# Performance work log

Hardware: AMD Instinct MI355X
Metric: run time of the kernel (lower is better)

The kernel has to match this reference:

```python
import jax, jax.numpy as jnp
import numpy as np

N = 50000
E = 800000
NEG_SLOPE = 0.2


def gat_layer(x, src, dst, W, al, ar):
    # x: [N, F_in]; W: [F_in, H*D]; al/ar: [H, D]
    H, D = al.shape
    feat = (x @ W).reshape(N, H, D)                      # [N, H, D]
    el = jnp.einsum('nhd,hd->nh', feat, al)              # [N, H]
    er = jnp.einsum('nhd,hd->nh', feat, ar)              # [N, H]
    e = jax.nn.leaky_relu(el[src] + er[dst], NEG_SLOPE)  # [E, H]
    # segment softmax over edges grouped by destination node
    m = jax.ops.segment_max(e, dst, num_segments=N)      # [N, H] (-inf for empty)
    a = jnp.exp(e - m[dst])                              # [E, H]
    s = jax.ops.segment_sum(a, dst, num_segments=N)      # [N, H]
    a = a / jnp.where(s[dst] > 0, s[dst], 1.0)
    # weighted gather-aggregate of messages
    out = jax.ops.segment_sum(a[:, :, None] * feat[src], dst, num_segments=N)
    return out                                           # [N, H, D]


def setup_inputs() -> dict:
    key = jax.random.key(0)
    ks = jax.random.split(key, 9)
    in_size, hid, out_size = 512, 64, 64
    H1, H2 = 4, 4
    return {
        'x':   jax.random.normal(ks[0], (N, in_size), dtype=jnp.float32),
        'src': jax.random.randint(ks[1], (E,), 0, N, dtype=jnp.int32),
        'dst': jax.random.randint(ks[2], (E,), 0, N, dtype=jnp.int32),
        'W1':  jax.random.normal(ks[3], (in_size, H1 * hid), dtype=jnp.float32) * 0.05,
        'al1': jax.random.normal(ks[4], (H1, hid), dtype=jnp.float32) * 0.1,
        'ar1': jax.random.normal(ks[5], (H1, hid), dtype=jnp.float32) * 0.1,
        'W2':  jax.random.normal(ks[6], (H1 * hid, H2 * out_size), dtype=jnp.float32) * 0.05,
        'al2': jax.random.normal(ks[7], (H2, out_size), dtype=jnp.float32) * 0.1,
        'ar2': jax.random.normal(ks[8], (H2, out_size), dtype=jnp.float32) * 0.1,
    }


def reference(x, src, dst, W1, al1, ar1, W2, al2, ar2):
    h = gat_layer(x, src, dst, W1, al1, ar1)   # [N, H1, hid]
    h = jax.nn.elu(h).reshape(N, -1)           # flatten heads -> [N, H1*hid]
    h = gat_layer(h, src, dst, W2, al2, ar2)   # [N, H2, out]
    return h.mean(axis=1)                      # mean over heads -> [N, out]
```

## Files before the change

### kernel.cpp

```cpp
#include <hip/hip_runtime.h>

#define NNODES 50000
#define NEDGES 800000
#define HH 4
#define DD 64
#define FEAT 256
#define MPAD 50048
#define NB 196
#define GB (MPAD / 128)
#define SB1 ((NEDGES + 511) / 512)
#define BCAP 128

typedef __attribute__((ext_vector_type(8))) _Float16 frag16;
typedef __attribute__((ext_vector_type(4))) float frag_cd;
typedef __attribute__((ext_vector_type(4))) _Float16 h4v;
typedef __attribute__((ext_vector_type(8))) _Float16 h8v;

__global__ __launch_bounds__(256) void front0_kernel(
    int* __restrict__ cnt, const float* __restrict__ W1,
    const float* __restrict__ W2, _Float16* __restrict__ Bp1,
    _Float16* __restrict__ Bp2) {
  int b = blockIdx.x;
  if (b < NB) {
    int i = b * 256 + threadIdx.x;
    if (i < NNODES) cnt[i] = 0;
  } else {
    int idx = (b - NB) * 256 + threadIdx.x;
    if (idx < 512 * 256) {
      int k = idx >> 8, n = idx & 255;
      Bp1[(size_t)n * 512 + k] = (_Float16)W1[idx];
    } else {
      idx -= 512 * 256;
      int k = idx >> 8, n = idx & 255;
      Bp2[(size_t)n * 256 + k] = (_Float16)W2[idx];
    }
  }
}

template <int AF32>
__device__ __forceinline__ void gemm_body(
    const void* __restrict__ Av, const _Float16* __restrict__ Bp,
    _Float16* __restrict__ featb, const float* __restrict__ al,
    const float* __restrict__ ar, float* __restrict__ elp,
    float* __restrict__ erp, int M, int K, int bid,
    _Float16* __restrict__ As, _Float16* __restrict__ Bs) {
  const int tid = threadIdx.x;
  const int w = tid >> 6, lane = tid & 63;
  const int q = lane >> 4, ln = lane & 15;
  const int rowBase = bid * 128;
  const int wm = (w >> 2) * 64;
  const int wn = (w & 3) * 64;

  frag_cd acc[4][4] = {};

  const int nt = K >> 6;
  const int srow8 = lane >> 3;
  const int scg = ((lane & 7) ^ srow8) * 8;
  const int sw = ln & 7;

  const int ar_ = tid >> 2, aq = tid & 3;
  const int as0 = ((aq * 2) ^ (ar_ & 7)) * 8;
  const int as1 = ((aq * 2 + 1) ^ (ar_ & 7)) * 8;
  const int xrow = rowBase + ar_;

  const float* __restrict__ x = (const float*)Av;
  const _Float16* __restrict__ Ap = (const _Float16*)Av;

  for (int t = 0; t < nt; ++t) {
    const int kk = t << 6;
    __syncthreads();

    if constexpr (AF32) {
      float4 v0, v1, v2, v3;
      v0 = v1 = v2 = v3 = make_float4(0.f, 0.f, 0.f, 0.f);
      if (xrow < M) {
        const float4* xp = (const float4*)(x + (size_t)xrow * 512 + kk + aq * 16);
        v0 = xp[0]; v1 = xp[1]; v2 = xp[2]; v3 = xp[3];
      }
      frag16 f0, f1;
      f0[0] = (_Float16)v0.x; f0[1] = (_Float16)v0.y;
      f0[2] = (_Float16)v0.z; f0[3] = (_Float16)v0.w;
      f0[4] = (_Float16)v1.x; f0[5] = (_Float16)v1.y;
      f0[6] = (_Float16)v1.z; f0[7] = (_Float16)v1.w;
      f1[0] = (_Float16)v2.x; f1[1] = (_Float16)v2.y;
      f1[2] = (_Float16)v2.z; f1[3] = (_Float16)v2.w;
      f1[4] = (_Float16)v3.x; f1[5] = (_Float16)v3.y;
      f1[6] = (_Float16)v3.z; f1[7] = (_Float16)v3.w;
      *(frag16*)&As[ar_ * 64 + as0] = f0;
      *(frag16*)&As[ar_ * 64 + as1] = f1;
    } else {
#pragma unroll
      for (int j = 0; j < 2; ++j) {
        int rloc = w * 16 + j * 8 + srow8;
        __builtin_amdgcn_global_load_lds(
            (const __attribute__((address_space(1))) void*)(Ap + (size_t)(rowBase + rloc) * K + kk + scg),
            (__attribute__((address_space(3))) void*)(&As[(w * 16 + j * 8) * 64 + lane * 8]), 16, 0, 0);
      }
    }
#pragma unroll
    for (int j = 0; j < 4; ++j) {
      int rloc = w * 32 + j * 8 + srow8;
      __builtin_amdgcn_global_load_lds(
          (const __attribute__((address_space(1))) void*)(Bp + (size_t)rloc * K + kk + scg),
          (__attribute__((address_space(3))) void*)(&Bs[(w * 32 + j * 8) * 64 + lane * 8]), 16, 0, 0);
    }
    __syncthreads();

#pragma unroll
    for (int ksub = 0; ksub < 2; ++ksub) {
      const int slot = ((ksub * 4 + q) ^ sw) * 8;
      frag16 a[4], b[4];
#pragma unroll
      for (int i = 0; i < 4; ++i)
        a[i] = *(const frag16*)&As[(wm + i * 16 + ln) * 64 + slot];
#pragma unroll
      for (int j = 0; j < 4; ++j)
        b[j] = *(const frag16*)&Bs[(wn + j * 16 + ln) * 64 + slot];
#pragma unroll
      for (int i = 0; i < 4; ++i)
#pragma unroll
        for (int j = 0; j < 4; ++j)
          acc[i][j] = __builtin_amdgcn_mfma_f32_16x16x32_f16(a[i], b[j], acc[i][j], 0, 0, 0);
    }
  }

#pragma unroll
  for (int i = 0; i < 4; ++i) {
    int rowg = rowBase + wm + i * 16 + q * 4;
#pragma unroll
    for (int r = 0; r < 4; ++r) {
      int row = rowg + r;
      if (row < M) {
#pragma unroll
        for (int j = 0; j < 4; ++j) {
          int col = wn + j * 16 + ln;
          featb[(size_t)row * 256 + col] = (_Float16)acc[i][j][r];
        }
      }
    }
  }

  const int h = wn >> 6;
  float alv[4], arv[4];
#pragma unroll
  for (int j = 0; j < 4; ++j) {
    alv[j] = al[h * DD + j * 16 + ln];
    arv[j] = ar[h * DD + j * 16 + ln];
  }
#pragma unroll
  for (int i = 0; i < 4; ++i) {
#pragma unroll
    for (int r = 0; r < 4; ++r) {
      float pl = 0.f, pr = 0.f;
#pragma unroll
      for (int j = 0; j < 4; ++j) {
        pl = fmaf(acc[i][j][r], alv[j], pl);
        pr = fmaf(acc[i][j][r], arv[j], pr);
      }
#pragma unroll
      for (int msk = 1; msk < 16; msk <<= 1) {
        pl += __shfl_xor(pl, msk);
        pr += __shfl_xor(pr, msk);
      }
      int row = rowBase + wm + i * 16 + q * 4 + r;
      if (ln == 0 && row < M) {
        elp[row * HH + h] = pl;
        erp[row * HH + h] = pr;
      }
    }
  }
}

__global__ __launch_bounds__(512) void fat1_kernel(
    const float* __restrict__ x, const _Float16* __restrict__ Bp1,
    _Float16* __restrict__ featb, const float* __restrict__ al,
    const float* __restrict__ ar, float* __restrict__ elp,
    float* __restrict__ erp, const int* __restrict__ src,
    const int* __restrict__ dst, int* __restrict__ cnt,
    int* __restrict__ bucket) {
  __shared__ _Float16 As[128 * 64];
  __shared__ _Float16 Bs[256 * 64];
  if (blockIdx.x < GB) {
    gemm_body<1>(x, Bp1, featb, al, ar, elp, erp, NNODES, 512, blockIdx.x, As, Bs);
  } else {
    int e = (blockIdx.x - GB) * 512 + threadIdx.x;
    if (e < NEDGES) {
      int d = dst[e];
      int pos = atomicAdd(&cnt[d], 1);
      if (pos < BCAP) bucket[(size_t)d * BCAP + pos] = src[e];
    }
  }
}

__global__ __launch_bounds__(512) void mfma_gemm2_kernel(
    const _Float16* __restrict__ Ap, const _Float16* __restrict__ Bp,
    _Float16* __restrict__ featb, const float* __restrict__ al,
    const float* __restrict__ ar, float* __restrict__ elp,
    float* __restrict__ erp) {
  __shared__ _Float16 As[128 * 64];
  __shared__ _Float16 Bs[256 * 64];
  gemm_body<0>(Ap, Bp, featb, al, ar, elp, erp, NNODES, 256, blockIdx.x, As, Bs);
}

template <int LAYER>
__global__ __launch_bounds__(256) void gat_agg_kernel(
    const int* __restrict__ cnt, const int* __restrict__ bucket,
    const float* __restrict__ el, const float* __restrict__ er,
    const _Float16* __restrict__ featb, float* __restrict__ outp,
    _Float16* __restrict__ outs) {
  __shared__ float sA[4][HH][68];
  __shared__ int sS[4][64];
  const int w = threadIdx.x >> 6;
  const int lane = threadIdx.x & 63;
  const int n = blockIdx.x * 4 + w;
  const int beg = n * BCAP;
  int deg = cnt[n];
  if (deg > BCAP) deg = BCAP;

  const int half = lane >> 5;
  const int fl = lane & 31;
  const int fb = fl << 3;
  const int hh = fl >> 3;

  float acc[8] = {0.f, 0.f, 0.f, 0.f, 0.f, 0.f, 0.f, 0.f};

  if (deg > 0 && deg <= 64) {
    const int h1 = lane & 3, j1 = lane >> 2;
    const float erd = er[n * HH + h1];
    float e[4], a[4];
    float m = -INFINITY;
#pragma unroll
    for (int p = 0; p < 4; ++p) {
      int j = j1 + p * 16;
      int s = 0;
      float ev = -INFINITY;
      if (j < deg) {
        s = bucket[beg + j];
        ev = el[s * HH + h1] + erd;
        ev = ev > 0.f ? ev : 0.2f * ev;
      }
      if (h1 == 0) sS[w][j] = s;
      e[p] = ev;
      m = fmaxf(m, ev);
    }
#pragma unroll
    for (int msk = 4; msk <= 32; msk <<= 1) m = fmaxf(m, __shfl_xor(m, msk));
    float ps = 0.f;
#pragma unroll
    for (int p = 0; p < 4; ++p) {
      a[p] = (j1 + p * 16 < deg) ? __expf(e[p] - m) : 0.f;
      ps += a[p];
    }
#pragma unroll
    for (int msk = 4; msk <= 32; msk <<= 1) ps += __shfl_xor(ps, msk);
    const float sinv = 1.f / ps;
#pragma unroll
    for (int p = 0; p < 4; ++p) {
      int j = j1 + p * 16;
      sA[w][h1][j] = a[p] * sinv;
    }

    const int deg2 = (deg + 1) & ~1;
    int j = 0;
    for (; j + 8 <= deg2; j += 8) {
      int s0 = sS[w][j + half];
      int s1 = sS[w][j + 2 + half];
      int s2 = sS[w][j + 4 + half];
      int s3 = sS[w][j + 6 + half];
      float a0 = sA[w][hh][j + half];
      float a1 = sA[w][hh][j + 2 + half];
      float a2 = sA[w][hh][j + 4 + half];
      float a3 = sA[w][hh][j + 6 + half];
      h8v u0 = *(const h8v*)&featb[(size_t)s0 * FEAT + fb];
      h8v u1 = *(const h8v*)&featb[(size_t)s1 * FEAT + fb];
      h8v u2 = *(const h8v*)&featb[(size_t)s2 * FEAT + fb];
      h8v u3 = *(const h8v*)&featb[(size_t)s3 * FEAT + fb];
#pragma unroll
      for (int c = 0; c < 8; ++c) acc[c] = fmaf(a0, (float)u0[c], acc[c]);
#pragma unroll
      for (int c = 0; c < 8; ++c) acc[c] = fmaf(a1, (float)u1[c], acc[c]);
#pragma unroll
      for (int c = 0; c < 8; ++c) acc[c] = fmaf(a2, (float)u2[c], acc[c]);
#pragma unroll
      for (int c = 0; c < 8; ++c) acc[c] = fmaf(a3, (float)u3[c], acc[c]);
    }
    for (; j < deg2; j += 2) {
      int s0 = sS[w][j + half];
      float a0 = sA[w][hh][j + half];
      h8v u0 = *(const h8v*)&featb[(size_t)s0 * FEAT + fb];
#pragma unroll
      for (int c = 0; c < 8; ++c) acc[c] = fmaf(a0, (float)u0[c], acc[c]);
    }
  } else if (deg > 64) {
    const int h1 = lane & 3, j1 = lane >> 2;
    const float erd = er[n * HH + h1];
    float m = -INFINITY;
    for (int j = j1; j < deg; j += 16) {
      int s = bucket[beg + j];
      float ev = el[s * HH + h1] + erd;
      ev = ev > 0.f ? ev : 0.2f * ev;
      m = fmaxf(m, ev);
    }
#pragma unroll
    for (int msk = 4; msk <= 32; msk <<= 1) m = fmaxf(m, __shfl_xor(m, msk));
    float ps = 0.f;
    for (int j = j1; j < deg; j += 16) {
      int s = bucket[beg + j];
      float ev = el[s * HH + h1] + erd;
      ev = ev > 0.f ? ev : 0.2f * ev;
      ps += __expf(ev - m);
    }
#pragma unroll
    for (int msk = 4; msk <= 32; msk <<= 1) ps += __shfl_xor(ps, msk);
    const float m2 = __shfl(m, hh);
    const float psinv2 = 1.f / __shfl(ps, hh);
    const float erd2 = er[n * HH + hh];
    for (int j = half; j < deg; j += 2) {
      int s = bucket[beg + j];
      float ev = el[s * HH + hh] + erd2;
      ev = ev > 0.f ? ev : 0.2f * ev;
      float a0 = __expf(ev - m2) * psinv2;
      h8v u0 = *(const h8v*)&featb[(size_t)s * FEAT + fb];
#pragma unroll
      for (int c = 0; c < 8; ++c) acc[c] = fmaf(a0, (float)u0[c], acc[c]);
    }
  }

#pragma unroll
  for (int c = 0; c < 8; ++c) acc[c] += __shfl_xor(acc[c], 32);

  if (LAYER == 1) {
    if (half == 0) {
      h8v o;
#pragma unroll
      for (int c = 0; c < 8; ++c) {
        float v = acc[c];
        v = v > 0.f ? v : (__expf(v) - 1.f);
        o[c] = (_Float16)v;
      }
      *(h8v*)&outs[(size_t)n * 256 + fb] = o;
    }
  } else {
#pragma unroll
    for (int c = 0; c < 8; ++c) {
      acc[c] += __shfl_xor(acc[c], 8);
      acc[c] += __shfl_xor(acc[c], 16);
    }
    if (lane < 8) {
      float4 o1 = make_float4(0.25f * acc[0], 0.25f * acc[1],
                              0.25f * acc[2], 0.25f * acc[3]);
      float4 o2 = make_float4(0.25f * acc[4], 0.25f * acc[5],
                              0.25f * acc[6], 0.25f * acc[7]);
      *(float4*)&outp[(size_t)n * DD + (lane << 3)] = o1;
      *(float4*)&outp[(size_t)n * DD + (lane << 3) + 4] = o2;
    }
  }
}

extern "C" void kernel_launch(void* const* d_in, const int* in_sizes, int n_in,
                              void* d_out, int out_size, void* d_ws, size_t ws_size,
                              hipStream_t stream) {
  const float* x   = (const float*)d_in[0];
  const int*   src = (const int*)d_in[1];
  const int*   dst = (const int*)d_in[2];
  const float* W1  = (const float*)d_in[3];
  const float* al1 = (const float*)d_in[4];
  const float* ar1 = (const float*)d_in[5];
  const float* W2  = (const float*)d_in[6];
  const float* al2 = (const float*)d_in[7];
  const float* ar2 = (const float*)d_in[8];
  float* out = (float*)d_out;

  float* ws = (float*)d_ws;
  float* el = ws;
  float* er = el + NNODES * HH;
  int* cnt    = (int*)(er + NNODES * HH);
  int* bucket = cnt + NNODES;
  uintptr_t p = ((uintptr_t)(bucket + (size_t)NNODES * BCAP) + 63) & ~(uintptr_t)63;
  _Float16* featb = (_Float16*)p;
  _Float16* Apr = featb + (size_t)NNODES * 256;
  Apr = (_Float16*)(((uintptr_t)Apr + 63) & ~(uintptr_t)63);
  _Float16* Bpr1 = Apr + (size_t)MPAD * 256;
  _Float16* Bpr2 = Bpr1 + 256 * 512;

  front0_kernel<<<NB + 768, 256, 0, stream>>>(cnt, W1, W2, Bpr1, Bpr2);
  fat1_kernel<<<GB + SB1, 512, 0, stream>>>(x, Bpr1, featb, al1, ar1, el, er,
                                            src, dst, cnt, bucket);
  gat_agg_kernel<1><<<NNODES / 4, 256, 0, stream>>>(cnt, bucket, el, er, featb, nullptr, Apr);
  mfma_gemm2_kernel<<<GB, 512, 0, stream>>>(Apr, Bpr2, featb, al2, ar2, el, er);
  gat_agg_kernel<2><<<NNODES / 4, 256, 0, stream>>>(cnt, bucket, el, er, featb, out, nullptr);
}
```

Before: 381.1 us.

## Store edge buckets as 16-bit indices and move scatter into front kernel

```diff
diff --git a/kernel.cpp b/kernel.cpp
--- a/kernel.cpp
+++ b/kernel.cpp
@@ -6,9 +6,9 @@
 #define DD 64
 #define FEAT 256
 #define MPAD 50048
-#define NB 196
 #define GB (MPAD / 128)
-#define SB1 ((NEDGES + 511) / 512)
+#define SCB ((NEDGES + 511) / 512)
+#define WPB 384
 #define BCAP 128
 
 typedef __attribute__((ext_vector_type(8))) _Float16 frag16;
@@ -16,20 +16,25 @@
 typedef __attribute__((ext_vector_type(4))) _Float16 h4v;
 typedef __attribute__((ext_vector_type(8))) _Float16 h8v;
 
-__global__ __launch_bounds__(256) void front0_kernel(
-    int* __restrict__ cnt, const float* __restrict__ W1,
-    const float* __restrict__ W2, _Float16* __restrict__ Bp1,
-    _Float16* __restrict__ Bp2) {
+__global__ __launch_bounds__(512) void front_kernel(
+    const int* __restrict__ src, const int* __restrict__ dst,
+    int* __restrict__ cnt, unsigned short* __restrict__ bucket,
+    const float* __restrict__ W1, const float* __restrict__ W2,
+    _Float16* __restrict__ Bp1, _Float16* __restrict__ Bp2) {
   int b = blockIdx.x;
-  if (b < NB) {
-    int i = b * 256 + threadIdx.x;
-    if (i < NNODES) cnt[i] = 0;
+  if (b < SCB) {
+    int e = b * 512 + threadIdx.x;
+    if (e < NEDGES) {
+      int d = dst[e];
+      int pos = atomicAdd(&cnt[d], 1);
+      if (pos < BCAP) bucket[(size_t)d * BCAP + pos] = (unsigned short)src[e];
+    }
   } else {
-    int idx = (b - NB) * 256 + threadIdx.x;
+    int idx = (b - SCB) * 512 + threadIdx.x;
     if (idx < 512 * 256) {
       int k = idx >> 8, n = idx & 255;
       Bp1[(size_t)n * 512 + k] = (_Float16)W1[idx];
-    } else {
+    } else if (idx < 768 * 256) {
       idx -= 512 * 256;
       int k = idx >> 8, n = idx & 255;
       Bp2[(size_t)n * 256 + k] = (_Float16)W2[idx];
@@ -171,25 +176,14 @@
   }
 }
 
-__global__ __launch_bounds__(512) void fat1_kernel(
-    const float* __restrict__ x, const _Float16* __restrict__ Bp1,
+__global__ __launch_bounds__(512) void mfma_gemm1_kernel(
+    const float* __restrict__ x, const _Float16* __restrict__ Bp,
     _Float16* __restrict__ featb, const float* __restrict__ al,
     const float* __restrict__ ar, float* __restrict__ elp,
-    float* __restrict__ erp, const int* __restrict__ src,
-    const int* __restrict__ dst, int* __restrict__ cnt,
-    int* __restrict__ bucket) {
+    float* __restrict__ erp) {
   __shared__ _Float16 As[128 * 64];
   __shared__ _Float16 Bs[256 * 64];
-  if (blockIdx.x < GB) {
-    gemm_body<1>(x, Bp1, featb, al, ar, elp, erp, NNODES, 512, blockIdx.x, As, Bs);
-  } else {
-    int e = (blockIdx.x - GB) * 512 + threadIdx.x;
-    if (e < NEDGES) {
-      int d = dst[e];
-      int pos = atomicAdd(&cnt[d], 1);
-      if (pos < BCAP) bucket[(size_t)d * BCAP + pos] = src[e];
-    }
-  }
+  gemm_body<1>(x, Bp, featb, al, ar, elp, erp, NNODES, 512, blockIdx.x, As, Bs);
 }
 
 __global__ __launch_bounds__(512) void mfma_gemm2_kernel(
@@ -204,7 +198,7 @@
 
 template <int LAYER>
 __global__ __launch_bounds__(256) void gat_agg_kernel(
-    const int* __restrict__ cnt, const int* __restrict__ bucket,
+    const int* __restrict__ cnt, const unsigned short* __restrict__ bucket,
     const float* __restrict__ el, const float* __restrict__ er,
     const _Float16* __restrict__ featb, float* __restrict__ outp,
     _Float16* __restrict__ outs) {
@@ -375,7 +369,7 @@
   float* el = ws;
   float* er = el + NNODES * HH;
   int* cnt    = (int*)(er + NNODES * HH);
-  int* bucket = cnt + NNODES;
+  unsigned short* bucket = (unsigned short*)(cnt + NNODES);
   uintptr_t p = ((uintptr_t)(bucket + (size_t)NNODES * BCAP) + 63) & ~(uintptr_t)63;
   _Float16* featb = (_Float16*)p;
   _Float16* Apr = featb + (size_t)NNODES * 256;
@@ -383,9 +377,9 @@
   _Float16* Bpr1 = Apr + (size_t)MPAD * 256;
   _Float16* Bpr2 = Bpr1 + 256 * 512;
 
-  front0_kernel<<<NB + 768, 256, 0, stream>>>(cnt, W1, W2, Bpr1, Bpr2);
-  fat1_kernel<<<GB + SB1, 512, 0, stream>>>(x, Bpr1, featb, al1, ar1, el, er,
-                                            src, dst, cnt, bucket);
+  hipMemsetAsync(cnt, 0, NNODES * sizeof(int), stream);
+  front_kernel<<<SCB + WPB, 512, 0, stream>>>(src, dst, cnt, bucket, W1, W2, Bpr1, Bpr2);
+  mfma_gemm1_kernel<<<GB, 512, 0, stream>>>(x, Bpr1, featb, al1, ar1, el, er);
   gat_agg_kernel<1><<<NNODES / 4, 256, 0, stream>>>(cnt, bucket, el, er, featb, nullptr, Apr);
   mfma_gemm2_kernel<<<GB, 512, 0, stream>>>(Apr, Bpr2, featb, al2, ar2, el, er);
   gat_agg_kernel<2><<<NNODES / 4, 256, 0, stream>>>(cnt, bucket, el, er, featb, out, nullptr);
```

Result: slower. 404.2 us (+6.0%).
